# Performance work log

Measured on AMD Instinct MI355X. Metric: run time of the kernel, lower is better.

Reference implementation:

```python
import jax, jax.numpy as jnp
import numpy as np

B, N, D = 16, 1024, 16  # graphs, nodes, embedding_dim


def setup_inputs() -> dict:
    key = jax.random.key(0)
    ks = jax.random.split(key, 13)
    s = 0.05  # small weight scale to keep exp(alpha) well-behaved
    return {
        "X": jax.random.normal(ks[0], (B, N, D), dtype=jnp.float32),
        "init_param": jax.random.normal(ks[1], (2,), dtype=jnp.float32) * s,
        "Wq": jax.random.normal(ks[2], (D - 1, D, D), dtype=jnp.float32) * s,
        "bq": jax.random.normal(ks[3], (D - 1, D), dtype=jnp.float32) * s,
        "Wk": jax.random.normal(ks[4], (D - 1, D, D), dtype=jnp.float32) * s,
        "bk": jax.random.normal(ks[5], (D - 1, D), dtype=jnp.float32) * s,
        "Wv": jax.random.normal(ks[6], (D - 1, D, D), dtype=jnp.float32) * s,
        "bv": jax.random.normal(ks[7], (D - 1, D), dtype=jnp.float32) * s,
        "Wo": jax.random.normal(ks[8], (D - 1, D, D), dtype=jnp.float32) * s,
        "bo": jax.random.normal(ks[9], (D - 1, D), dtype=jnp.float32) * s,
        "Wf": jax.random.normal(ks[10], (D - 1, 2, D), dtype=jnp.float32) * s,
        "bf": jax.random.normal(ks[11], (D - 1, 2), dtype=jnp.float32) * s,
    }


def reference(X, init_param, Wq, bq, Wk, bk, Wv, bv, Wo, bo, Wf, bf):
    b, n, d = X.shape
    dt = X.dtype
    Zs = []
    logdet = jnp.zeros((b, n), dt)
    for i in range(d):
        if i == 0:
            mu, alpha = init_param[0], init_param[1]
        else:
            l = i - 1
            Xi = X[:, :, :i]  # [B,N,i] growing ragged slice
            Q = Xi @ Wq[l, :i, :i].T + bq[l, :i]
            K = Xi @ Wk[l, :i, :i].T + bk[l, :i]
            V = Xi @ Wv[l, :i, :i].T + bv[l, :i]
            # SAB/MAB: softmax(QK^T / sqrt(dim_V=i)); num_heads=1
            A = jax.nn.softmax(
                jnp.einsum("bnd,bmd->bnm", Q, K) / jnp.sqrt(jnp.asarray(i, dt)),
                axis=-1,
            )  # [B,N,N]
            O = Q + jnp.einsum("bnm,bmd->bnd", A, V)
            O = O + jax.nn.relu(O @ Wo[l, :i, :i].T + bo[l, :i])
            out = O @ Wf[l, :, :i].T + bf[l]  # [B,N,2]
            mu, alpha = out[..., 0], out[..., 1]
        Zs.append((X[:, :, i] - mu) / jnp.exp(alpha))
        logdet = logdet - alpha
    Z = jnp.stack(Zs, axis=-1)
    return Z, logdet
```

## Files before the change

kernel.cpp:

```cpp
#include <hip/hip_runtime.h>
#include <math.h>

#define Bb 16
#define Nn 1024
#define Dd 16
#define NL 15

typedef __attribute__((ext_vector_type(8))) short short8;
typedef __attribute__((ext_vector_type(4))) float f32x4;
typedef __attribute__((ext_vector_type(16))) float f32x16;

#if __has_builtin(__builtin_amdgcn_exp2f)
#define EXP2(x) __builtin_amdgcn_exp2f(x)
#else
#define EXP2(x) exp2f(x)
#endif

#define VSTR 1040
#define PSTR 40
#define WREG (64 * PSTR * 2)
#define V_OFF (Nn * Dd * 2)
#define P_OFF (V_OFF + Dd * VSTR * 2)
#define LDS_TOTAL (P_OFF + 16 * WREG)

__device__ __forceinline__ unsigned pack2bf(float a, float b) {
    unsigned ua = __float_as_uint(a) + 0x8000u;
    unsigned ub = __float_as_uint(b) + 0x8000u;
    return (ua >> 16) | (ub & 0xffff0000u);
}
__device__ __forceinline__ unsigned short bf1(float a) {
    return (unsigned short)((__float_as_uint(a) + 0x8000u) >> 16);
}

__device__ __forceinline__ void project(const float* __restrict__ xrow,
                                        const float* __restrict__ W,
                                        const float* __restrict__ bias,
                                        int i, float* __restrict__ q) {
#pragma unroll
    for (int r = 0; r < 16; r++) q[r] = 0.f;
    for (int c = 0; c < i; c++) {
        float xc = xrow[c];
#pragma unroll
        for (int r = 0; r < 16; r++) q[r] = fmaf(xc, W[r * 16 + c], q[r]);
    }
#pragma unroll
    for (int r = 0; r < 16; r++) q[r] = (r < i) ? (q[r] + bias[r]) : 0.f;
}

__device__ __forceinline__ void load_row16(const float* __restrict__ p, float* __restrict__ x) {
    const float4* xp = (const float4*)p;
    float4 a = xp[0], b = xp[1], c = xp[2], d = xp[3];
    x[0]=a.x; x[1]=a.y; x[2]=a.z; x[3]=a.w;
    x[4]=b.x; x[5]=b.y; x[6]=b.z; x[7]=b.w;
    x[8]=c.x; x[9]=c.y; x[10]=c.z; x[11]=c.w;
    x[12]=d.x; x[13]=d.y; x[14]=d.z; x[15]=d.w;
}

__launch_bounds__(1024, 4)
__global__ void gf_fused(const float* __restrict__ X,
                         const float* __restrict__ Wq, const float* __restrict__ bq,
                         const float* __restrict__ Wk, const float* __restrict__ bk,
                         const float* __restrict__ Wv, const float* __restrict__ bv,
                         const float* __restrict__ Wo, const float* __restrict__ bo,
                         const float* __restrict__ Wf, const float* __restrict__ bf,
                         float* __restrict__ als, float* __restrict__ out) {
    extern __shared__ char smem[];
    const int l = blockIdx.x, b = blockIdx.y, i = l + 1;
    const int t = threadIdx.x;
    const int wid = t >> 6, lane = t & 63;
    const int c15 = lane & 15, quad = lane >> 4;
    const int q31 = lane & 31, h = lane >> 5;
    const float qscale = 1.4426950408889634f * rsqrtf((float)i);

    unsigned short* Ksh = (unsigned short*)smem;
    unsigned short* Vsh = (unsigned short*)(smem + V_OFF);
    unsigned short* Pw  = (unsigned short*)(smem + P_OFF + wid * WREG);

    const float* Xb  = X  + (size_t)b * Nn * Dd;
    const float* wq  = Wq + l * 256;  const float* bql = bq + l * 16;
    const float* wk  = Wk + l * 256;  const float* bkl = bk + l * 16;
    const float* wvp = Wv + l * 256;  const float* bvl = bv + l * 16;
    const float* wo  = Wo + l * 256;  const float* bol = bo + l * 16;
    const float* wf  = Wf + l * 32;   const float* bfl = bf + l * 2;

    {
        float xr[16]; load_row16(Xb + (size_t)t * Dd, xr);
        float tmp[16];
        unsigned u[8];

        project(xr, wk, bkl, i, tmp);
#pragma unroll
        for (int r = 0; r < 8; r++) u[r] = pack2bf(tmp[2*r], tmp[2*r+1]);
        {
            uint4* kd = (uint4*)(Ksh + t * 16);
            kd[0] = make_uint4(u[0], u[1], u[2], u[3]);
            kd[1] = make_uint4(u[4], u[5], u[6], u[7]);
        }

        project(xr, wvp, bvl, i, tmp);
#pragma unroll
        for (int d = 0; d < 16; d++) Vsh[d * VSTR + t] = bf1(tmp[d]);

        project(xr, wq, bql, i, tmp);
#pragma unroll
        for (int r = 0; r < 8; r++) u[r] = pack2bf(tmp[2*r] * qscale, tmp[2*r+1] * qscale);
        {
            uint4* qd = (uint4*)(Pw + lane * PSTR);
            qd[0] = make_uint4(u[0], u[1], u[2], u[3]);
            qd[1] = make_uint4(u[4], u[5], u[6], u[7]);
        }
    }
    __syncthreads();

    f32x16 zf16 = {};
    f32x4  zf4  = {};

    short8 qf[2];
    qf[0] = *(const short8*)(Pw + q31        * PSTR + h * 8);
    qf[1] = *(const short8*)(Pw + (32 + q31) * PSTR + h * 8);

    const unsigned short* Kp = Ksh + (size_t)q31 * 16 + h * 8;
    const unsigned short* Vp = Vsh + (size_t)c15 * VSTR + quad * 8;

    f32x4 ot[4] = {zf4, zf4, zf4, zf4};
    float rs[2] = {0.f, 0.f};

    short8 kf = *(const short8*)(Kp);
    short8 vf = *(const short8*)(Vp);

    for (int kb = 0; kb < Nn; kb += 32) {
        const int kn = (kb + 32) & (Nn - 1);
        short8 kfn = *(const short8*)(Kp + (size_t)kn * 16);
        short8 vfn = *(const short8*)(Vp + kn);

        f32x16 st0 = __builtin_amdgcn_mfma_f32_32x32x16_bf16(kf, qf[0], zf16, 0, 0, 0);
        f32x16 st1 = __builtin_amdgcn_mfma_f32_32x32x16_bf16(kf, qf[1], zf16, 0, 0, 0);

        unsigned short* pw0 = Pw + q31 * PSTR + 4 * h;
#pragma unroll
        for (int g = 0; g < 4; g++) {
            float e0 = EXP2(st0[4*g+0]), e1 = EXP2(st0[4*g+1]);
            float e2 = EXP2(st0[4*g+2]), e3 = EXP2(st0[4*g+3]);
            rs[0] += (e0 + e1) + (e2 + e3);
            *(uint2*)(pw0 + 8*g) = make_uint2(pack2bf(e0, e1), pack2bf(e2, e3));
        }
        unsigned short* pw1 = pw0 + 32 * PSTR;
#pragma unroll
        for (int g = 0; g < 4; g++) {
            float e0 = EXP2(st1[4*g+0]), e1 = EXP2(st1[4*g+1]);
            float e2 = EXP2(st1[4*g+2]), e3 = EXP2(st1[4*g+3]);
            rs[1] += (e0 + e1) + (e2 + e3);
            *(uint2*)(pw1 + 8*g) = make_uint2(pack2bf(e0, e1), pack2bf(e2, e3));
        }

#pragma unroll
        for (int f = 0; f < 4; f++) {
            short8 pf = *(const short8*)(Pw + (f*16 + c15) * PSTR + quad * 8);
            ot[f] = __builtin_amdgcn_mfma_f32_16x16x32_bf16(vf, pf, ot[f], 0, 0, 0);
        }
        kf = kfn; vf = vfn;
    }

    rs[0] += __shfl_xor(rs[0], 32);
    rs[1] += __shfl_xor(rs[1], 32);
    const float iv0 = 1.f / rs[0];
    const float iv1 = 1.f / rs[1];

    float* Ow = (float*)Pw;
#pragma unroll
    for (int f = 0; f < 4; f++) {
        float iv = __shfl((f & 2) ? iv1 : iv0, (f & 1) * 16 + c15);
        f32x4 res;
        res.x = ot[f].x * iv; res.y = ot[f].y * iv;
        res.z = ot[f].z * iv; res.w = ot[f].w * iv;
        *(f32x4*)(Ow + (f*16 + c15) * 20 + quad * 4) = res;
    }

    {
        float xr[16]; load_row16(Xb + (size_t)t * Dd, xr);
        float q[16];  project(xr, wq, bql, i, q);
        const float* orow = (const float*)(smem + P_OFF + wid * WREG) + lane * 20;

        float a[16];
#pragma unroll
        for (int c = 0; c < 16; c++) a[c] = q[c] + orow[c];

        float tt[16];
#pragma unroll
        for (int r = 0; r < 16; r++) {
            float acc = bol[r];
#pragma unroll
            for (int c = 0; c < 16; c++) acc = fmaf(a[c], wo[r * 16 + c], acc);
            tt[r] = fmaxf(acc, 0.f);
        }
#pragma unroll
        for (int r = 0; r < 16; r++) a[r] += (r < i) ? tt[r] : 0.f;

        float mu = bfl[0], al = bfl[1];
#pragma unroll
        for (int c = 0; c < 16; c++) {
            mu = fmaf(a[c], wf[c], mu);
            al = fmaf(a[c], wf[16 + c], al);
        }
        out[((size_t)(b * Nn + t)) * Dd + i] = (xr[i] - mu) * __expf(-al);
        als[(size_t)l * (Bb * Nn) + b * Nn + t] = al;
    }
}

__launch_bounds__(1024)
__global__ void gf_final(const float* __restrict__ X, const float* __restrict__ ip,
                         const float* __restrict__ als, float* __restrict__ out) {
    const int idx = blockIdx.x * 1024 + threadIdx.x;
    const float mu = ip[0], a0 = ip[1];
    float x0 = X[(size_t)idx * Dd];
    out[(size_t)idx * Dd] = (x0 - mu) * __expf(-a0);
    float ld = -a0;
#pragma unroll
    for (int l = 0; l < NL; l++) ld -= als[(size_t)l * (Bb * Nn) + idx];
    out[(size_t)Bb * Nn * Dd + idx] = ld;
}

__global__ void gf_init(const float* __restrict__ X, const float* __restrict__ ip,
                        float* __restrict__ out) {
    int idx = blockIdx.x * blockDim.x + threadIdx.x;
    if (idx >= Bb * Nn) return;
    float mu = ip[0], alpha = ip[1];
    float x0 = X[(size_t)idx * Dd];
    out[(size_t)idx * Dd] = (x0 - mu) * __expf(-alpha);
    out[(size_t)Bb * Nn * Dd + idx] = -alpha;
}

__launch_bounds__(512, 2)
__global__ void gf_layer_fb(const float* __restrict__ X,
                            const float* __restrict__ Wq, const float* __restrict__ bq,
                            const float* __restrict__ Wk, const float* __restrict__ bk,
                            const float* __restrict__ Wv, const float* __restrict__ bv,
                            const float* __restrict__ Wo, const float* __restrict__ bo,
                            const float* __restrict__ Wf, const float* __restrict__ bf,
                            float* __restrict__ out) {
    const int l = blockIdx.x, b = blockIdx.y, i = l + 1, t = threadIdx.x;
    const float rscale = rsqrtf((float)i);
    __shared__ float Ksh[512 * 16];
    __shared__ float Vsh[512 * 16];
    const float* Xb = X + (size_t)b * Nn * Dd;
    const float* wq = Wq + l * 256; const float* wk = Wk + l * 256;
    const float* wv = Wv + l * 256; const float* wo = Wo + l * 256;
    const float* wf = Wf + l * 32;
    const float* bql = bq + l * 16; const float* bkl = bk + l * 16;
    const float* bvl = bv + l * 16; const float* bol = bo + l * 16;
    const float* bfl = bf + l * 2;
    const int n0 = t, n1 = t + 512;
    float q0[16], q1[16], xi0, xi1;
    {
        float xr[16];
        load_row16(Xb + (size_t)n0 * Dd, xr); xi0 = xr[i]; project(xr, wq, bql, i, q0);
        load_row16(Xb + (size_t)n1 * Dd, xr); xi1 = xr[i]; project(xr, wq, bql, i, q1);
    }
    float o0[16], o1[16];
#pragma unroll
    for (int c = 0; c < 16; c++) { o0[c] = 0.f; o1[c] = 0.f; }
    float ls0 = 0.f, ls1 = 0.f;
    for (int ch = 0; ch < 2; ch++) {
        float kr[16], vr[16];
        {
            float kx[16];
            load_row16(Xb + (size_t)(ch * 512 + t) * Dd, kx);
            project(kx, wk, bkl, i, kr);
            project(kx, wv, bvl, i, vr);
        }
        __syncthreads();
#pragma unroll
        for (int j = 0; j < 4; j++) {
            ((float4*)&Ksh[t * 16])[j] = ((float4*)kr)[j];
            ((float4*)&Vsh[t * 16])[j] = ((float4*)vr)[j];
        }
        __syncthreads();
        for (int k = 0; k < 512; k++) {
            float kk[16], vv[16];
#pragma unroll
            for (int j = 0; j < 4; j++) ((float4*)kk)[j] = ((const float4*)&Ksh[k * 16])[j];
            float s0 = 0.f, s1 = 0.f;
#pragma unroll
            for (int c = 0; c < 16; c++) { s0 = fmaf(q0[c], kk[c], s0); s1 = fmaf(q1[c], kk[c], s1); }
            float p0 = __expf(s0 * rscale), p1 = __expf(s1 * rscale);
            ls0 += p0; ls1 += p1;
#pragma unroll
            for (int j = 0; j < 4; j++) ((float4*)vv)[j] = ((const float4*)&Vsh[k * 16])[j];
#pragma unroll
            for (int c = 0; c < 16; c++) { o0[c] = fmaf(p0, vv[c], o0[c]); o1[c] = fmaf(p1, vv[c], o1[c]); }
        }
        __syncthreads();
    }
    float* logdet = out + (size_t)Bb * Nn * Dd;
#pragma unroll
    for (int rowsel = 0; rowsel < 2; rowsel++) {
        const float* qr = rowsel ? q1 : q0; const float* orr = rowsel ? o1 : o0;
        float lsum = rowsel ? ls1 : ls0; float xin = rowsel ? xi1 : xi0;
        int n = rowsel ? n1 : n0;
        float a[16]; float inv = 1.f / lsum;
#pragma unroll
        for (int c = 0; c < 16; c++) a[c] = qr[c] + orr[c] * inv;
        float tt[16];
#pragma unroll
        for (int r = 0; r < 16; r++) {
            float acc = bol[r];
#pragma unroll
            for (int c = 0; c < 16; c++) acc = fmaf(a[c], wo[r * 16 + c], acc);
            tt[r] = fmaxf(acc, 0.f);
        }
#pragma unroll
        for (int r = 0; r < 16; r++) a[r] += (r < i) ? tt[r] : 0.f;
        float mu = bfl[0], al = bfl[1];
#pragma unroll
        for (int c = 0; c < 16; c++) { mu = fmaf(a[c], wf[c], mu); al = fmaf(a[c], wf[16 + c], al); }
        out[((size_t)(b * Nn + n)) * Dd + i] = (xin - mu) * __expf(-al);
        atomicAdd(logdet + b * Nn + n, -al);
    }
}

extern "C" void kernel_launch(void* const* d_in, const int* in_sizes, int n_in,
                              void* d_out, int out_size, void* d_ws, size_t ws_size,
                              hipStream_t stream) {
    const float* X  = (const float*)d_in[0];
    const float* ip = (const float*)d_in[1];
    const float* Wq = (const float*)d_in[2];
    const float* bq = (const float*)d_in[3];
    const float* Wk = (const float*)d_in[4];
    const float* bk = (const float*)d_in[5];
    const float* Wv = (const float*)d_in[6];
    const float* bv = (const float*)d_in[7];
    const float* Wo = (const float*)d_in[8];
    const float* bo = (const float*)d_in[9];
    const float* Wf = (const float*)d_in[10];
    const float* bf = (const float*)d_in[11];
    float* out = (float*)d_out;

    const size_t need = (size_t)NL * Bb * Nn * sizeof(float);
    hipError_t e = hipFuncSetAttribute((const void*)gf_fused,
                                       hipFuncAttributeMaxDynamicSharedMemorySize,
                                       LDS_TOTAL);
    if (e == hipSuccess && ws_size >= need) {
        float* als = (float*)d_ws;
        gf_fused<<<dim3(NL, Bb), 1024, LDS_TOTAL, stream>>>(
            X, Wq, bq, Wk, bk, Wv, bv, Wo, bo, Wf, bf, als, out);
        gf_final<<<Bb, 1024, 0, stream>>>(X, ip, als, out);
    } else {
        gf_init<<<(Bb * Nn + 255) / 256, 256, 0, stream>>>(X, ip, out);
        gf_layer_fb<<<dim3(NL, Bb), 512, 0, stream>>>(
            X, Wq, bq, Wk, bk, Wv, bv, Wo, bo, Wf, bf, out);
    }
}
```

Before: 156.3 us.

## Keep softmax probabilities in registers and use 32x32 MFMA for PV

Moves the P@V product out of LDS. The exponentiated scores are packed into bf16 registers and fed straight into 32x32x16 MFMAs as the A operand, with V read as the B operand. This removes the per-iteration LDS write and read of P and the per-wave P scratch region, and Q fragments are now built with cross-lane shuffles instead of an LDS round trip. In exchange there is an extra block-wide barrier, the output is staged through the reused K region, and only half of the 32 output columns carry useful data, which wastes some MFMA throughput.

```diff
diff --git a/kernel.cpp b/kernel.cpp
--- a/kernel.cpp
+++ b/kernel.cpp
@@ -9,6 +9,7 @@
 typedef __attribute__((ext_vector_type(8))) short short8;
 typedef __attribute__((ext_vector_type(4))) float f32x4;
 typedef __attribute__((ext_vector_type(16))) float f32x16;
+typedef __attribute__((ext_vector_type(4))) unsigned uint4v;
 
 #if __has_builtin(__builtin_amdgcn_exp2f)
 #define EXP2(x) __builtin_amdgcn_exp2f(x)
@@ -16,12 +17,10 @@
 #define EXP2(x) exp2f(x)
 #endif
 
-#define VSTR 1040
-#define PSTR 40
-#define WREG (64 * PSTR * 2)
-#define V_OFF (Nn * Dd * 2)
-#define P_OFF (V_OFF + Dd * VSTR * 2)
-#define LDS_TOTAL (P_OFF + 16 * WREG)
+#define VSTR 1044
+#define V_OFF 32768
+#define RS_OFF 65536
+#define LDS_TOTAL 69632
 
 __device__ __forceinline__ unsigned pack2bf(float a, float b) {
     unsigned ua = __float_as_uint(a) + 0x8000u;
@@ -68,13 +67,11 @@
     const int l = blockIdx.x, b = blockIdx.y, i = l + 1;
     const int t = threadIdx.x;
     const int wid = t >> 6, lane = t & 63;
-    const int c15 = lane & 15, quad = lane >> 4;
     const int q31 = lane & 31, h = lane >> 5;
     const float qscale = 1.4426950408889634f * rsqrtf((float)i);
 
     unsigned short* Ksh = (unsigned short*)smem;
     unsigned short* Vsh = (unsigned short*)(smem + V_OFF);
-    unsigned short* Pw  = (unsigned short*)(smem + P_OFF + wid * WREG);
 
     const float* Xb  = X  + (size_t)b * Nn * Dd;
     const float* wq  = Wq + l * 256;  const float* bql = bq + l * 16;
@@ -83,6 +80,7 @@
     const float* wo  = Wo + l * 256;  const float* bol = bo + l * 16;
     const float* wf  = Wf + l * 32;   const float* bfl = bf + l * 2;
 
+    unsigned qu[8];
     {
         float xr[16]; load_row16(Xb + (size_t)t * Dd, xr);
         float tmp[16];
@@ -103,87 +101,102 @@
 
         project(xr, wq, bql, i, tmp);
 #pragma unroll
-        for (int r = 0; r < 8; r++) u[r] = pack2bf(tmp[2*r] * qscale, tmp[2*r+1] * qscale);
-        {
-            uint4* qd = (uint4*)(Pw + lane * PSTR);
-            qd[0] = make_uint4(u[0], u[1], u[2], u[3]);
-            qd[1] = make_uint4(u[4], u[5], u[6], u[7]);
-        }
+        for (int r = 0; r < 8; r++) qu[r] = pack2bf(tmp[2*r] * qscale, tmp[2*r+1] * qscale);
     }
     __syncthreads();
 
+    short8 qf0, qf1;
+    {
+        unsigned d0[4], d1[4];
+#pragma unroll
+        for (int j = 0; j < 4; j++) {
+            unsigned lo = __shfl(qu[j], q31);
+            unsigned hi = __shfl(qu[4 + j], q31);
+            d0[j] = h ? hi : lo;
+            lo = __shfl(qu[j], 32 + q31);
+            hi = __shfl(qu[4 + j], 32 + q31);
+            d1[j] = h ? hi : lo;
+        }
+        uint4v v0 = {d0[0], d0[1], d0[2], d0[3]};
+        uint4v v1 = {d1[0], d1[1], d1[2], d1[3]};
+        qf0 = __builtin_bit_cast(short8, v0);
+        qf1 = __builtin_bit_cast(short8, v1);
+    }
+
     f32x16 zf16 = {};
-    f32x4  zf4  = {};
-
-    short8 qf[2];
-    qf[0] = *(const short8*)(Pw + q31        * PSTR + h * 8);
-    qf[1] = *(const short8*)(Pw + (32 + q31) * PSTR + h * 8);
-
-    const unsigned short* Kp = Ksh + (size_t)q31 * 16 + h * 8;
-    const unsigned short* Vp = Vsh + (size_t)c15 * VSTR + quad * 8;
-
-    f32x4 ot[4] = {zf4, zf4, zf4, zf4};
-    float rs[2] = {0.f, 0.f};
-
-    short8 kf = *(const short8*)(Kp);
-    short8 vf = *(const short8*)(Vp);
+    f32x16 D0 = {}, D1 = {};
+    float rs0 = 0.f, rs1 = 0.f;
+
+    const unsigned short* Kp   = Ksh + (size_t)q31 * 16 + h * 8;
+    const unsigned short* Vrow = Vsh + (size_t)(q31 & 15) * VSTR;
+
+    short8 kf = *(const short8*)Kp;
 
     for (int kb = 0; kb < Nn; kb += 32) {
-        const int kn = (kb + 32) & (Nn - 1);
-        short8 kfn = *(const short8*)(Kp + (size_t)kn * 16);
-        short8 vfn = *(const short8*)(Vp + kn);
-
-        f32x16 st0 = __builtin_amdgcn_mfma_f32_32x32x16_bf16(kf, qf[0], zf16, 0, 0, 0);
-        f32x16 st1 = __builtin_amdgcn_mfma_f32_32x32x16_bf16(kf, qf[1], zf16, 0, 0, 0);
-
-        unsigned short* pw0 = Pw + q31 * PSTR + 4 * h;
+        short8 kfn = *(const short8*)(Kp + (size_t)((kb + 32) & (Nn - 1)) * 16);
+
+        f32x16 s0 = __builtin_amdgcn_mfma_f32_32x32x16_bf16(kf, qf0, zf16, 0, 0, 0);
+        f32x16 s1 = __builtin_amdgcn_mfma_f32_32x32x16_bf16(kf, qf1, zf16, 0, 0, 0);
+        kf = kfn;
+
+        unsigned p0[8], p1[8];
 #pragma unroll
         for (int g = 0; g < 4; g++) {
-            float e0 = EXP2(st0[4*g+0]), e1 = EXP2(st0[4*g+1]);
-            float e2 = EXP2(st0[4*g+2]), e3 = EXP2(st0[4*g+3]);
-            rs[0] += (e0 + e1) + (e2 + e3);
-            *(uint2*)(pw0 + 8*g) = make_uint2(pack2bf(e0, e1), pack2bf(e2, e3));
-        }
-        unsigned short* pw1 = pw0 + 32 * PSTR;
+            float e0 = EXP2(s0[4*g+0]), e1 = EXP2(s0[4*g+1]);
+            float e2 = EXP2(s0[4*g+2]), e3 = EXP2(s0[4*g+3]);
+            rs0 += (e0 + e1) + (e2 + e3);
+            p0[2*g]   = pack2bf(e0, e1);
+            p0[2*g+1] = pack2bf(e2, e3);
+        }
 #pragma unroll
         for (int g = 0; g < 4; g++) {
-            float e0 = EXP2(st1[4*g+0]), e1 = EXP2(st1[4*g+1]);
-            float e2 = EXP2(st1[4*g+2]), e3 = EXP2(st1[4*g+3]);
-            rs[1] += (e0 + e1) + (e2 + e3);
-            *(uint2*)(pw1 + 8*g) = make_uint2(pack2bf(e0, e1), pack2bf(e2, e3));
-        }
-
-#pragma unroll
-        for (int f = 0; f < 4; f++) {
-            short8 pf = *(const short8*)(Pw + (f*16 + c15) * PSTR + quad * 8);
-            ot[f] = __builtin_amdgcn_mfma_f32_16x16x32_bf16(vf, pf, ot[f], 0, 0, 0);
-        }
-        kf = kfn; vf = vfn;
-    }
-
-    rs[0] += __shfl_xor(rs[0], 32);
-    rs[1] += __shfl_xor(rs[1], 32);
-    const float iv0 = 1.f / rs[0];
-    const float iv1 = 1.f / rs[1];
-
-    float* Ow = (float*)Pw;
-#pragma unroll
-    for (int f = 0; f < 4; f++) {
-        float iv = __shfl((f & 2) ? iv1 : iv0, (f & 1) * 16 + c15);
-        f32x4 res;
-        res.x = ot[f].x * iv; res.y = ot[f].y * iv;
-        res.z = ot[f].z * iv; res.w = ot[f].w * iv;
-        *(f32x4*)(Ow + (f*16 + c15) * 20 + quad * 4) = res;
-    }
+            float e0 = EXP2(s1[4*g+0]), e1 = EXP2(s1[4*g+1]);
+            float e2 = EXP2(s1[4*g+2]), e3 = EXP2(s1[4*g+3]);
+            rs1 += (e0 + e1) + (e2 + e3);
+            p1[2*g]   = pack2bf(e0, e1);
+            p1[2*g+1] = pack2bf(e2, e3);
+        }
+
+#pragma unroll
+        for (int s = 0; s < 2; s++) {
+            const unsigned short* vb = Vrow + kb + 16*s + 4*h;
+            uint2 va = *(const uint2*)vb;
+            uint2 vc = *(const uint2*)(vb + 8);
+            uint4v vv = {va.x, va.y, vc.x, vc.y};
+            short8 vf = __builtin_bit_cast(short8, vv);
+            uint4v a0 = {p0[4*s], p0[4*s+1], p0[4*s+2], p0[4*s+3]};
+            uint4v a1 = {p1[4*s], p1[4*s+1], p1[4*s+2], p1[4*s+3]};
+            D0 = __builtin_amdgcn_mfma_f32_32x32x16_bf16(__builtin_bit_cast(short8, a0), vf, D0, 0, 0, 0);
+            D1 = __builtin_amdgcn_mfma_f32_32x32x16_bf16(__builtin_bit_cast(short8, a1), vf, D1, 0, 0, 0);
+        }
+    }
+
+    rs0 += __shfl_xor(rs0, 32);
+    rs1 += __shfl_xor(rs1, 32);
+
+    __syncthreads();
+
+    float* Ow = (float*)smem + wid * 1024;
+    if (q31 < 16) {
+#pragma unroll
+        for (int r = 0; r < 16; r++) {
+            int m = (r & 3) + 8 * (r >> 2) + 4 * h;
+            Ow[m * 16 + q31]        = D0[r];
+            Ow[(m + 32) * 16 + q31] = D1[r];
+        }
+    }
+    float* Rw = (float*)(smem + RS_OFF) + wid * 64;
+    if (h == 0) { Rw[q31] = rs0; Rw[32 + q31] = rs1; }
 
     {
         float xr[16]; load_row16(Xb + (size_t)t * Dd, xr);
         float q[16];  project(xr, wq, bql, i, q);
-        const float* orow = (const float*)(smem + P_OFF + wid * WREG) + lane * 20;
+        const float* orow = (const float*)smem + wid * 1024 + lane * 16;
+        const float  inv  = 1.f / Rw[lane];
 
         float a[16];
 #pragma unroll
-        for (int c = 0; c < 16; c++) a[c] = q[c] + orow[c];
+        for (int c = 0; c < 16; c++) a[c] = q[c] + orow[c] * inv;
 
         float tt[16];
 #pragma unroll
```

Result: no change. 155.5 us (-0.5%).
